# Kernel tuning notes

Measured on AMD Instinct MI355X. Metric: run time of the kernel, lower is better.

## Reference

```python
import jax, jax.numpy as jnp
import numpy as np

L = 8          # curve control points per chunk (self.l)
TS = 256       # curve spatial resolution (self.ts)


def setup_inputs() -> dict:
    key = jax.random.key(0)
    k1, k2 = jax.random.split(key)
    # full-resolution input image, values in [0,1)
    x = jax.random.uniform(k1, (4, 3, 1024, 1024), dtype=jnp.float32)
    # predicted curve parameters: 9*L = 72 channels at TS x TS
    param = jax.random.normal(k2, (4, 72, TS, TS), dtype=jnp.float32)
    return {"x": x, "param": param}


def _grid_sample_3d(vol, gx, gy, gz):
    """F.grid_sample(vol, grid, 'bilinear', 'border', align_corners=True)
    vol: [B,C,D,Hc,Wc]; gx,gy,gz: [B,H,W] normalized coords in [-1,1].
    Returns [B,H,W,C] (channels last)."""
    B, C, D, Hc, Wc = vol.shape
    # align_corners=True unnormalization + border padding (clamp coords)
    ix = jnp.clip((gx + 1.0) * 0.5 * (Wc - 1), 0.0, Wc - 1)
    iy = jnp.clip((gy + 1.0) * 0.5 * (Hc - 1), 0.0, Hc - 1)
    iz = jnp.clip((gz + 1.0) * 0.5 * (D - 1), 0.0, D - 1)
    x0f, y0f, z0f = jnp.floor(ix), jnp.floor(iy), jnp.floor(iz)
    wx, wy, wz = ix - x0f, iy - y0f, iz - z0f
    x0 = x0f.astype(jnp.int32); x1 = jnp.minimum(x0 + 1, Wc - 1)
    y0 = y0f.astype(jnp.int32); y1 = jnp.minimum(y0 + 1, Hc - 1)
    z0 = z0f.astype(jnp.int32); z1 = jnp.minimum(z0 + 1, D - 1)
    vol_t = vol.transpose(0, 2, 3, 4, 1)  # [B,D,Hc,Wc,C]
    b = jnp.arange(B)[:, None, None]      # [B,1,1]
    out = jnp.zeros(gx.shape + (C,), dtype=vol.dtype)
    for zi, wz_ in ((z0, 1.0 - wz), (z1, wz)):
        for yi, wy_ in ((y0, 1.0 - wy), (y1, wy)):
            for xi, wx_ in ((x0, 1.0 - wx), (x1, wx)):
                w = (wz_ * wy_ * wx_)[..., None]          # [B,H,W,1]
                out = out + w * vol_t[b, zi, yi, xi]      # gather -> [B,H,W,C]
    return out


def reference(x, param):
    # eval-mode forward of Generator.mapping + tanh (param precomputed by CNN)
    B, _, H, W = x.shape
    Hc, Wc = param.shape[-2], param.shape[-1]
    # torch.stack(torch.chunk(param,3,dim=1),dim=1) == reshape [B,3,3L,Hc,Wc]
    curve = param.reshape(B, 3, 3 * L, Hc, Wc)
    coordh = jnp.linspace(-1.0, 1.0, H, dtype=x.dtype)[:, None]  # varies over H
    coordw = jnp.linspace(-1.0, 1.0, W, dtype=x.dtype)[None, :]  # varies over W
    gx = jnp.broadcast_to(coordw, (B, H, W))
    gy = jnp.broadcast_to(coordh, (B, H, W))
    out = jnp.zeros((B, H, W, 3), dtype=x.dtype)
    for i in range(3):  # three curve chunks, z-coordinate = i-th color channel
        curve_i = curve[:, :, i * L:(i + 1) * L]          # [B,3,L,Hc,Wc]
        out = out + _grid_sample_3d(curve_i, gx, gy, x[:, i])
    return jnp.tanh(out.transpose(0, 3, 1, 2))            # [B,3,H,W]
```

## Files before the change

### kernel.cpp

```cpp
#include <hip/hip_runtime.h>
#include <math.h>

#define IMG 1024
#define HW (IMG * IMG)
#define TS 256
#define CH_STRIDE (TS * TS)
#define PARAM_B_STRIDE (72 * CH_STRIDE)
#define S_CONST (255.0f / 1023.0f)

#define ROWS 3
#define CELLS 66
#define CELL_DW 77
#define ROW_DW (CELLS * CELL_DW)
#define LDS_DW (ROWS * ROW_DW)

__global__ __launch_bounds__(1024, 8) void curve3d_fused(
    const float* __restrict__ x, const float* __restrict__ param,
    float* __restrict__ out)
{
    __shared__ float sh[LDS_DW];
    int blk = blockIdx.x;
    int wt = blk & 3;
    int ht = (blk >> 2) & 255;
    int b  = blk >> 10;
    int tid = threadIdx.x;

    int w0 = wt * 256, h0 = ht * 4;
    int xb = (int)((float)w0 * S_CONST);
    int yb = (int)((float)h0 * S_CONST);

    int tw = tid & 255, th = tid >> 8;
    int w = w0 + tw, h = h0 + th;
    const float* xp = x + (size_t)b * 3 * HW + (size_t)h * IMG + w;
    float xv[3];
    xv[0] = xp[0]; xv[1] = xp[(size_t)HW]; xv[2] = xp[(size_t)2 * HW];

    int g = tid >> 6, u = tid & 63;
    const float* pb = param + (size_t)b * PARAM_B_STRIDE;
    int ys0 = min(yb, 255), ys1 = min(yb + 1, 255), ys2 = min(yb + 2, 255);
#pragma unroll
    for (int j = 0; j < 14; ++j) {
        int rid = j * 16 + g;
        if (rid < 216) {
            int row = (rid >= 144) ? 2 : ((rid >= 72) ? 1 : 0);
            int ch = rid - row * 72;
            int ys = (row == 2) ? ys2 : ((row == 1) ? ys1 : ys0);
            float v = pb[(size_t)ch * CH_STRIDE + ys * TS + (xb + u)];
            sh[row * ROW_DW + u * CELL_DW + ch] = v;
        }
    }
    if (tid < 432) {
        int rid = tid >> 1;
        int xx = 64 + (tid & 1);
        int row = (rid >= 144) ? 2 : ((rid >= 72) ? 1 : 0);
        int ch = rid - row * 72;
        int ys = (row == 2) ? ys2 : ((row == 1) ? ys1 : ys0);
        int xs = min(xb + xx, 255);
        sh[row * ROW_DW + xx * CELL_DW + ch] =
            pb[(size_t)ch * CH_STRIDE + ys * TS + xs];
    }

    int zi[3]; float wz[3];
#pragma unroll
    for (int i = 0; i < 3; ++i) {
        float izf = fminf(fmaxf(fmaf(xv[i], 3.5f, 3.5f), 0.0f), 7.0f);
        int z = min((int)izf, 6);
        zi[i] = z;
        wz[i] = izf - (float)z;
    }

    __syncthreads();

    float ix = (float)w * S_CONST; int x0 = (int)ix; float wx = ix - (float)x0;
    float iy = (float)h * S_CONST; int y0 = (int)iy; float wy = iy - (float)y0;
    int c0 = x0 - xb;
    int c1 = min(x0 + 1, 255) - xb;
    int r0 = y0 - yb;
    int r1 = min(y0 + 1, 255) - yb;

    float u0 = 1.0f - wx, v0 = 1.0f - wy;
    float wcs[4] = {v0 * u0, v0 * wx, wy * u0, wy * wx};
    const float* bases[4] = {
        sh + r0 * ROW_DW + c0 * CELL_DW,
        sh + r0 * ROW_DW + c1 * CELL_DW,
        sh + r1 * ROW_DW + c0 * CELL_DW,
        sh + r1 * ROW_DW + c1 * CELL_DW
    };

    float* op = out + (size_t)b * 3 * HW + (size_t)h * IMG + w;
#pragma unroll
    for (int c = 0; c < 3; ++c) {
        float acc = 0.0f;
#pragma unroll
        for (int i = 0; i < 3; ++i) {
            int off = (c * 3 + i) * 8 + zi[i];
            float wzi = wz[i];
#pragma unroll
            for (int k = 0; k < 4; ++k) {
                float2 v;
                __builtin_memcpy(&v, bases[k] + off, 8);
                float wb = wcs[k] * wzi;
                float wa = wcs[k] - wb;
                acc = fmaf(v.x, wa, fmaf(v.y, wb, acc));
            }
        }
        float e = __expf(2.0f * acc);
        op[(size_t)c * HW] = 1.0f - 2.0f / (e + 1.0f);
    }
}

extern "C" void kernel_launch(void* const* d_in, const int* in_sizes, int n_in,
                              void* d_out, int out_size, void* d_ws, size_t ws_size,
                              hipStream_t stream) {
    const float* x = (const float*)d_in[0];
    const float* param = (const float*)d_in[1];
    float* out = (float*)d_out;
    curve3d_fused<<<dim3(4 * 256 * 4), dim3(1024), 0, stream>>>(x, param, out);
}
```

Measured before the change: 186.9 us.

## Retile to 128x16 output blocks with two rows per thread and swizzled block order

New measurement: 181.2 us. 3.1% less time.

```diff
diff --git a/kernel.cpp b/kernel.cpp
--- a/kernel.cpp
+++ b/kernel.cpp
@@ -8,11 +8,13 @@
 #define PARAM_B_STRIDE (72 * CH_STRIDE)
 #define S_CONST (255.0f / 1023.0f)
 
-#define ROWS 3
-#define CELLS 66
-#define CELL_DW 77
+#define ROWS 6
+#define CELLS 34
+#define CELL_DW 73
 #define ROW_DW (CELLS * CELL_DW)
 #define LDS_DW (ROWS * ROW_DW)
+#define RUNS (ROWS * 72)
+#define STAGE_DW (RUNS * CELLS)
 
 __global__ __launch_bounds__(1024, 8) void curve3d_fused(
     const float* __restrict__ x, const float* __restrict__ param,
@@ -20,92 +22,93 @@
 {
     __shared__ float sh[LDS_DW];
     int blk = blockIdx.x;
-    int wt = blk & 3;
-    int ht = (blk >> 2) & 255;
-    int b  = blk >> 10;
+    blk = (blk & 7) * 256 + (blk >> 3);
+    int wt = blk & 7;
+    int ht = (blk >> 3) & 63;
+    int b  = blk >> 9;
     int tid = threadIdx.x;
 
-    int w0 = wt * 256, h0 = ht * 4;
+    int w0 = wt * 128, h0 = ht * 16;
     int xb = (int)((float)w0 * S_CONST);
     int yb = (int)((float)h0 * S_CONST);
 
-    int tw = tid & 255, th = tid >> 8;
-    int w = w0 + tw, h = h0 + th;
-    const float* xp = x + (size_t)b * 3 * HW + (size_t)h * IMG + w;
-    float xv[3];
-    xv[0] = xp[0]; xv[1] = xp[(size_t)HW]; xv[2] = xp[(size_t)2 * HW];
+    int tw = tid & 127, th = tid >> 7;
+    int w = w0 + tw;
+    int ha = h0 + th;
+    const float* xp = x + (size_t)b * 3 * HW + (size_t)ha * IMG + w;
+    float xv[2][3];
+#pragma unroll
+    for (int i = 0; i < 3; ++i) {
+        xv[0][i] = __builtin_nontemporal_load(xp + (size_t)i * HW);
+        xv[1][i] = __builtin_nontemporal_load(xp + (size_t)i * HW + 8 * IMG);
+    }
 
-    int g = tid >> 6, u = tid & 63;
     const float* pb = param + (size_t)b * PARAM_B_STRIDE;
-    int ys0 = min(yb, 255), ys1 = min(yb + 1, 255), ys2 = min(yb + 2, 255);
 #pragma unroll
-    for (int j = 0; j < 14; ++j) {
-        int rid = j * 16 + g;
-        if (rid < 216) {
-            int row = (rid >= 144) ? 2 : ((rid >= 72) ? 1 : 0);
-            int ch = rid - row * 72;
-            int ys = (row == 2) ? ys2 : ((row == 1) ? ys1 : ys0);
-            float v = pb[(size_t)ch * CH_STRIDE + ys * TS + (xb + u)];
-            sh[row * ROW_DW + u * CELL_DW + ch] = v;
+    for (int j = 0; j < 15; ++j) {
+        int idx = tid + j * 1024;
+        if (j < 14 || idx < STAGE_DW) {
+            int run = idx / CELLS;
+            int off = idx - run * CELLS;
+            int row = run / 72;
+            int ch  = run - row * 72;
+            int ys = min(yb + row, 255);
+            int xs = min(xb + off, 255);
+            sh[row * ROW_DW + off * CELL_DW + ch] =
+                pb[(size_t)ch * CH_STRIDE + ys * TS + xs];
         }
     }
-    if (tid < 432) {
-        int rid = tid >> 1;
-        int xx = 64 + (tid & 1);
-        int row = (rid >= 144) ? 2 : ((rid >= 72) ? 1 : 0);
-        int ch = rid - row * 72;
-        int ys = (row == 2) ? ys2 : ((row == 1) ? ys1 : ys0);
-        int xs = min(xb + xx, 255);
-        sh[row * ROW_DW + xx * CELL_DW + ch] =
-            pb[(size_t)ch * CH_STRIDE + ys * TS + xs];
-    }
 
-    int zi[3]; float wz[3];
+    int zi[2][3]; float wz[2][3];
 #pragma unroll
-    for (int i = 0; i < 3; ++i) {
-        float izf = fminf(fmaxf(fmaf(xv[i], 3.5f, 3.5f), 0.0f), 7.0f);
-        int z = min((int)izf, 6);
-        zi[i] = z;
-        wz[i] = izf - (float)z;
-    }
+    for (int p = 0; p < 2; ++p)
+#pragma unroll
+        for (int i = 0; i < 3; ++i) {
+            float f = fminf(fmaxf(fmaf(xv[p][i], 3.5f, 3.5f), 0.0f), 7.0f);
+            int z = min((int)f, 6);
+            zi[p][i] = z;
+            wz[p][i] = f - (float)z;
+        }
 
     __syncthreads();
 
-    float ix = (float)w * S_CONST; int x0 = (int)ix; float wx = ix - (float)x0;
-    float iy = (float)h * S_CONST; int y0 = (int)iy; float wy = iy - (float)y0;
-    int c0 = x0 - xb;
-    int c1 = min(x0 + 1, 255) - xb;
-    int r0 = y0 - yb;
-    int r1 = min(y0 + 1, 255) - yb;
+    float ixf = (float)w * S_CONST; int x0 = (int)ixf; float wx = ixf - (float)x0;
+    int cb0 = (x0 - xb) * CELL_DW;
+    int cb1 = (min(x0 + 1, 255) - xb) * CELL_DW;
+    float u0 = 1.0f - wx;
 
-    float u0 = 1.0f - wx, v0 = 1.0f - wy;
-    float wcs[4] = {v0 * u0, v0 * wx, wy * u0, wy * wx};
-    const float* bases[4] = {
-        sh + r0 * ROW_DW + c0 * CELL_DW,
-        sh + r0 * ROW_DW + c1 * CELL_DW,
-        sh + r1 * ROW_DW + c0 * CELL_DW,
-        sh + r1 * ROW_DW + c1 * CELL_DW
-    };
+    float* op = out + (size_t)b * 3 * HW + (size_t)ha * IMG + w;
 
-    float* op = out + (size_t)b * 3 * HW + (size_t)h * IMG + w;
 #pragma unroll
-    for (int c = 0; c < 3; ++c) {
-        float acc = 0.0f;
+    for (int p = 0; p < 2; ++p) {
+        int h = ha + p * 8;
+        float iyf = (float)h * S_CONST; int y0 = (int)iyf; float wy = iyf - (float)y0;
+        int rb0 = (y0 - yb) * ROW_DW;
+        int rb1 = (min(y0 + 1, 255) - yb) * ROW_DW;
+        float v0 = 1.0f - wy;
+        float wcs[4] = {v0 * u0, v0 * wx, wy * u0, wy * wx};
+        int bofs[4] = {rb0 + cb0, rb0 + cb1, rb1 + cb0, rb1 + cb1};
+        float* opp = op + (size_t)(p * 8) * IMG;
 #pragma unroll
-        for (int i = 0; i < 3; ++i) {
-            int off = (c * 3 + i) * 8 + zi[i];
-            float wzi = wz[i];
+        for (int c = 0; c < 3; ++c) {
+            float acc = 0.0f;
 #pragma unroll
-            for (int k = 0; k < 4; ++k) {
-                float2 v;
-                __builtin_memcpy(&v, bases[k] + off, 8);
-                float wb = wcs[k] * wzi;
-                float wa = wcs[k] - wb;
-                acc = fmaf(v.x, wa, fmaf(v.y, wb, acc));
+            for (int i = 0; i < 3; ++i) {
+                int off = (c * 3 + i) * 8 + zi[p][i];
+                float wzi = wz[p][i];
+#pragma unroll
+                for (int k = 0; k < 4; ++k) {
+                    float2 v;
+                    __builtin_memcpy(&v, &sh[bofs[k] + off], 8);
+                    float wb = wcs[k] * wzi;
+                    float wa = wcs[k] - wb;
+                    acc = fmaf(v.x, wa, fmaf(v.y, wb, acc));
+                }
             }
+            float e = __expf(2.0f * acc);
+            __builtin_nontemporal_store(1.0f - 2.0f / (e + 1.0f),
+                                        opp + (size_t)c * HW);
         }
-        float e = __expf(2.0f * acc);
-        op[(size_t)c * HW] = 1.0f - 2.0f / (e + 1.0f);
     }
 }
 
@@ -115,5 +118,5 @@
     const float* x = (const float*)d_in[0];
     const float* param = (const float*)d_in[1];
     float* out = (float*)d_out;
-    curve3d_fused<<<dim3(4 * 256 * 4), dim3(1024), 0, stream>>>(x, param, out);
+    curve3d_fused<<<dim3(4 * 64 * 8), dim3(1024), 0, stream>>>(x, param, out);
 }
```
